# Performance work log

Measured on AMD Instinct MI355X. Metric: run time of the kernel, lower is better.

Reference implementation:

```python
import jax, jax.numpy as jnp
import numpy as np

N_BLADES = 8

def _build_cayley():
    """Geometric-product table for Cl(3,0): C[i,j,k] s.t. (e_i * e_j) = sum_k C[i,j,k] e_k.
    Blade order: [1, e1, e2, e3, e12, e13, e23, e123] via bitmasks [0,1,2,4,3,5,6,7]."""
    blades = [0, 1, 2, 4, 3, 5, 6, 7]
    idx = {b: i for i, b in enumerate(blades)}
    C = np.zeros((8, 8, 8), dtype=np.float32)
    for i, a in enumerate(blades):
        for j, b in enumerate(blades):
            aa = a >> 1
            cnt = 0
            while aa:
                cnt += bin(aa & b).count('1')
                aa >>= 1
            sign = -1.0 if (cnt & 1) else 1.0
            C[i, j, idx[a ^ b]] += sign
    return jnp.asarray(C)

CAYLEY = _build_cayley()

def clifford_linear(x, w, b):
    # x: (..., 8), w: (8,), b: (8,) -> geometric product w * x + b
    return jnp.einsum('ijk,i,...j->...k', CAYLEY, w, x) + b

def setup_inputs() -> dict:
    key = jax.random.key(0)
    ks = jax.random.split(key, 9)
    B, S = 4, 4096
    inp = {'x': jax.random.normal(ks[0], (B, S, N_BLADES), dtype=jnp.float32)}
    names = ['wq', 'bq', 'wk', 'bk', 'wv', 'bv', 'wo', 'bo']
    for i, n in enumerate(names):
        scale = 1.0 / np.sqrt(N_BLADES) if n.startswith('w') else 0.02
        inp[n] = jax.random.normal(ks[i + 1], (N_BLADES,), dtype=jnp.float32) * scale
    return inp

def reference(x, wq, bq, wk, bk, wv, bv, wo, bo):
    # head_dim = max(1, 8 // 2) = 4 -> scale = sqrt(4) = 2
    scale = jnp.float32(2.0)
    Q = clifford_linear(x, wq, bq)  # (B,S,8)
    K = clifford_linear(x, wk, bk)
    V = clifford_linear(x, wv, bv)
    c0 = CAYLEY[..., 0]  # (8,8) scalar part of geometric product
    attn = jnp.einsum('ij,bsi,btj->bst', c0, Q, K) / scale  # (B,S,S)
    attn = jax.nn.softmax(attn, axis=-1)
    out = jnp.einsum('bst,btk->bsk', attn, V)  # (B,S,8)
    return clifford_linear(out, wo, bo)
```

## Files before the change

### kernel.cpp

```cpp
#include <hip/hip_runtime.h>
#include <math.h>

#define SEQ 4096
#define NBATCH 4
#define SGRP 64
#define TWAVES 16
#define TCHUNK (SEQ / TWAVES)
#define TT 32
#define VTILE 288

typedef _Float16 f16;
typedef __attribute__((ext_vector_type(8))) _Float16 f16x8;
typedef __attribute__((ext_vector_type(8))) __bf16 bf16x8;
typedef __attribute__((ext_vector_type(16))) float f32x16;
typedef __attribute__((ext_vector_type(4))) unsigned u32x4;
typedef __attribute__((ext_vector_type(2))) unsigned u32x2;

__device__ __forceinline__ float fexp2(float x) {
#if __has_builtin(__builtin_amdgcn_exp2f)
  return __builtin_amdgcn_exp2f(x);
#else
  return exp2f(x);
#endif
}

__device__ __forceinline__ u32x2 pswap(unsigned a, unsigned b) {
#if __has_builtin(__builtin_amdgcn_permlane32_swap)
  return __builtin_amdgcn_permlane32_swap(a, b, false, false);
#else
  asm volatile("v_permlane32_swap_b32 %0, %1" : "+v"(a), "+v"(b));
  u32x2 r; r[0] = a; r[1] = b; return r;
#endif
}

__device__ __forceinline__ unsigned exp2_pk_bf16(float a, float b) {
  unsigned e0 = __builtin_bit_cast(unsigned, fexp2(a));
  unsigned e1 = __builtin_bit_cast(unsigned, fexp2(b));
  return __builtin_amdgcn_perm(e1, e0, 0x07060302u);
}

__device__ __forceinline__ unsigned short f2bf(float f) {
  unsigned u = __builtin_bit_cast(unsigned, f);
  u += 0x7FFF + ((u >> 16) & 1);
  return (unsigned short)(u >> 16);
}

__device__ __forceinline__ float cl_sign(int amask, int bmask) {
  int cnt = 0, aa = amask >> 1;
  while (aa) { cnt += __popc(aa & bmask); aa >>= 1; }
  return (cnt & 1) ? -1.f : 1.f;
}

__global__ __launch_bounds__(256) void ck_qkv(const float* __restrict__ x,
                                              const float* __restrict__ wq,
                                              const float* __restrict__ bq,
                                              const float* __restrict__ wk,
                                              const float* __restrict__ bk,
                                              const float* __restrict__ wv,
                                              const float* __restrict__ bv,
                                              f16* __restrict__ Qp,
                                              f16* __restrict__ Kp,
                                              unsigned short* __restrict__ Vt) {
  __shared__ float Pl[288];
  const int blades[8] = {0, 1, 2, 4, 3, 5, 6, 7};
  int tid = threadIdx.x;

  if (tid < 64) {
    int j = tid >> 3, k = tid & 7;
    int bj = blades[j];
    float mq = 0.f, mk = 0.f, mv = 0.f;
    for (int i = 0; i < 8; ++i) {
      int ai = blades[i];
      if (blades[ai ^ bj] != k) continue;
      float sgn = cl_sign(ai, bj);
      mq += sgn * wq[i]; mk += sgn * wk[i]; mv += sgn * wv[i];
    }
    float c0 = cl_sign(blades[k], blades[k]);
    const float F = 0.72134752044448170368f;
    Pl[tid]       = mq * c0 * F;
    Pl[64 + tid]  = mk;
    Pl[128 + tid] = mv;
    if (j == 0) {
      Pl[256 + k] = bq[k] * c0 * F;
      Pl[264 + k] = bk[k];
      Pl[272 + k] = bv[k];
    }
  }
  __syncthreads();

  int gid = blockIdx.x * 256 + tid;
  int row = gid >> 3;
  int c = gid & 7;
  int b = row >> 12;
  int s = row & (SEQ - 1);
  const float4* x4 = (const float4*)(x + (size_t)row * 8);
  float4 xa = x4[0], xb = x4[1];
  float xr[8] = {xa.x, xa.y, xa.z, xa.w, xb.x, xb.y, xb.z, xb.w};
  float q = Pl[256 + c], k = Pl[264 + c], v = Pl[272 + c];
#pragma unroll
  for (int j = 0; j < 8; ++j) {
    q = fmaf(xr[j], Pl[j * 8 + c], q);
    k = fmaf(xr[j], Pl[64 + j * 8 + c], k);
    v = fmaf(xr[j], Pl[128 + j * 8 + c], v);
  }
  f16 qh = (f16)q;
  f16 ql = (f16)(q - (float)qh);
  Qp[(size_t)row * 16 + c] = qh;
  Qp[(size_t)row * 16 + 8 + c] = ql;
  Kp[(size_t)row * 8 + c] = (f16)k;
  unsigned short* vt = Vt + ((size_t)b * (SEQ / 32) + (s >> 5)) * VTILE + (s & 31);
  vt[c * 32] = f2bf(v);
  if (c == 0) vt[8 * 32] = 0x3F80;
}

__global__ __launch_bounds__(1024, 4) void ck_attn(const f16* __restrict__ Qp,
                                                   const f16* __restrict__ Kp,
                                                   const unsigned short* __restrict__ Vt,
                                                   const float* __restrict__ wo,
                                                   const float* __restrict__ bo,
                                                   float* __restrict__ out) {
  __shared__ float Lo[TWAVES][SGRP][9];
  __shared__ float MoL[72];

  const int tid = threadIdx.x;
  const int w = tid >> 6;
  const int lane = tid & 63;
  const int ls = lane & 31;
  const int hf = lane >> 5;
  const int rowbase = blockIdx.x * SGRP;
  const int b = rowbase >> 12;

  if (tid < 64) {
    const int blades[8] = {0, 1, 2, 4, 3, 5, 6, 7};
    int j = tid >> 3, k = tid & 7;
    int bj = blades[j];
    float mo = 0.f;
    for (int i = 0; i < 8; ++i) {
      int ai = blades[i];
      if (blades[ai ^ bj] != k) continue;
      mo += cl_sign(ai, bj) * wo[i];
    }
    MoL[tid] = mo;
    if (j == 0) MoL[64 + k] = bo[k];
  }

  f16x8 qf0 = *(const f16x8*)(Qp + (size_t)(rowbase + ls) * 16 + 8 * hf);
  f16x8 qf1 = *(const f16x8*)(Qp + (size_t)(rowbase + 32 + ls) * 16 + 8 * hf);

  f32x16 acc0 = {0.f, 0.f, 0.f, 0.f, 0.f, 0.f, 0.f, 0.f,
                 0.f, 0.f, 0.f, 0.f, 0.f, 0.f, 0.f, 0.f};
  f32x16 acc1 = acc0;
  const f32x16 zero = acc0;

  const f16* kbase = Kp + ((size_t)b * SEQ + w * TCHUNK + ls) * 8;
  const unsigned short* vbase =
      Vt + ((size_t)b * (SEQ / 32) + w * (TCHUNK / 32)) * VTILE +
      (ls <= 8 ? ls : 8) * 32 + 8 * hf;

  const int NIT = TCHUNK / TT;

#pragma unroll 1
  for (int it = 0; it < NIT; ++it) {
    const int t0 = it * TT;
    f16x8 kf = *(const f16x8*)(kbase + (size_t)t0 * 8);
    u32x4 v0 = *(const u32x4*)(vbase + (size_t)it * VTILE);
    u32x4 v1 = *(const u32x4*)(vbase + (size_t)it * VTILE + 16);

    f32x16 s0 = __builtin_amdgcn_mfma_f32_32x32x16_f16(kf, qf0, zero, 0, 0, 0);
    f32x16 s1 = __builtin_amdgcn_mfma_f32_32x32x16_f16(kf, qf1, zero, 0, 0, 0);

    unsigned a0 = exp2_pk_bf16(s0[0], s0[1]);
    unsigned b0 = exp2_pk_bf16(s1[0], s1[1]);
    unsigned a1 = exp2_pk_bf16(s0[2], s0[3]);
    unsigned b1 = exp2_pk_bf16(s1[2], s1[3]);
    unsigned a2 = exp2_pk_bf16(s0[4], s0[5]);
    unsigned b2 = exp2_pk_bf16(s1[4], s1[5]);
    unsigned a3 = exp2_pk_bf16(s0[6], s0[7]);
    unsigned b3 = exp2_pk_bf16(s1[6], s1[7]);
    u32x2 ra02 = pswap(a0, a2);
    u32x2 rb02 = pswap(b0, b2);
    u32x2 ra13 = pswap(a1, a3);
    u32x2 rb13 = pswap(b1, b3);
    u32x4 pa0 = {ra02[0], ra13[0], ra02[1], ra13[1]};
    u32x4 pb0 = {rb02[0], rb13[0], rb02[1], rb13[1]};
    acc0 = __builtin_amdgcn_mfma_f32_32x32x16_bf16(
        __builtin_bit_cast(bf16x8, v0), __builtin_bit_cast(bf16x8, pa0), acc0, 0, 0, 0);
    acc1 = __builtin_amdgcn_mfma_f32_32x32x16_bf16(
        __builtin_bit_cast(bf16x8, v0), __builtin_bit_cast(bf16x8, pb0), acc1, 0, 0, 0);

    unsigned a4 = exp2_pk_bf16(s0[8], s0[9]);
    unsigned b4 = exp2_pk_bf16(s1[8], s1[9]);
    unsigned a5 = exp2_pk_bf16(s0[10], s0[11]);
    unsigned b5 = exp2_pk_bf16(s1[10], s1[11]);
    unsigned a6 = exp2_pk_bf16(s0[12], s0[13]);
    unsigned b6 = exp2_pk_bf16(s1[12], s1[13]);
    unsigned a7 = exp2_pk_bf16(s0[14], s0[15]);
    unsigned b7 = exp2_pk_bf16(s1[14], s1[15]);
    u32x2 ra46 = pswap(a4, a6);
    u32x2 rb46 = pswap(b4, b6);
    u32x2 ra57 = pswap(a5, a7);
    u32x2 rb57 = pswap(b5, b7);
    u32x4 pa1 = {ra46[0], ra57[0], ra46[1], ra57[1]};
    u32x4 pb1 = {rb46[0], rb57[0], rb46[1], rb57[1]};
    acc0 = __builtin_amdgcn_mfma_f32_32x32x16_bf16(
        __builtin_bit_cast(bf16x8, v1), __builtin_bit_cast(bf16x8, pa1), acc0, 0, 0, 0);
    acc1 = __builtin_amdgcn_mfma_f32_32x32x16_bf16(
        __builtin_bit_cast(bf16x8, v1), __builtin_bit_cast(bf16x8, pb1), acc1, 0, 0, 0);
  }

  if (hf == 0) {
    Lo[w][ls][0] = acc0[0]; Lo[w][ls][1] = acc0[1];
    Lo[w][ls][2] = acc0[2]; Lo[w][ls][3] = acc0[3];
    Lo[w][ls][8] = acc0[4];
    Lo[w][32 + ls][0] = acc1[0]; Lo[w][32 + ls][1] = acc1[1];
    Lo[w][32 + ls][2] = acc1[2]; Lo[w][32 + ls][3] = acc1[3];
    Lo[w][32 + ls][8] = acc1[4];
  } else {
    Lo[w][ls][4] = acc0[0]; Lo[w][ls][5] = acc0[1];
    Lo[w][ls][6] = acc0[2]; Lo[w][ls][7] = acc0[3];
    Lo[w][32 + ls][4] = acc1[0]; Lo[w][32 + ls][5] = acc1[1];
    Lo[w][32 + ls][6] = acc1[2]; Lo[w][32 + ls][7] = acc1[3];
  }
  __syncthreads();

  if (tid < SGRP * 9) {
    int s = tid / 9, j = tid - s * 9;
    float sum = 0.f;
#pragma unroll
    for (int w2 = 0; w2 < TWAVES; ++w2) sum += Lo[w2][s][j];
    Lo[0][s][j] = sum;
  }
  __syncthreads();

  if (tid < SGRP * 8) {
    int s = tid >> 3, ko = tid & 7;
    float inv = 1.f / Lo[0][s][8];
    float a = MoL[64 + ko];
#pragma unroll
    for (int j = 0; j < 8; ++j) a = fmaf(Lo[0][s][j] * inv, MoL[j * 8 + ko], a);
    out[(size_t)(rowbase + s) * 8 + ko] = a;
  }
}

extern "C" void kernel_launch(void* const* d_in, const int* in_sizes, int n_in,
                              void* d_out, int out_size, void* d_ws, size_t ws_size,
                              hipStream_t stream) {
  const float* x  = (const float*)d_in[0];
  const float* wq = (const float*)d_in[1];
  const float* bq = (const float*)d_in[2];
  const float* wk = (const float*)d_in[3];
  const float* bk = (const float*)d_in[4];
  const float* wv = (const float*)d_in[5];
  const float* bv = (const float*)d_in[6];
  const float* wo = (const float*)d_in[7];
  const float* bo = (const float*)d_in[8];

  f16* Qp = (f16*)d_ws;
  f16* Kp = Qp + (size_t)NBATCH * SEQ * 16;
  unsigned short* Vt = (unsigned short*)(Kp + (size_t)NBATCH * SEQ * 8);
  float* outp = (float*)d_out;

  hipLaunchKernelGGL(ck_qkv, dim3(NBATCH * SEQ * 8 / 256), dim3(256), 0, stream,
                     x, wq, bq, wk, bk, wv, bv, Qp, Kp, Vt);
  hipLaunchKernelGGL(ck_attn, dim3(NBATCH * SEQ / SGRP), dim3(1024), 0, stream,
                     Qp, Kp, Vt, wo, bo, outp);
}
```

Baseline: 21.02 us.

## Fuse QKV projection and attention into one cooperative kernel with grid sync

Merges the QKV projection kernel and the attention kernel into a single cooperative launch of 256 blocks. Each block first projects its own 64 rows into Q, K and V in the workspace, then waits on a grid-wide barrier before running attention. This removes one kernel launch and the gap between the two kernels. In exchange it adds the cost of a grid-wide sync and a cooperative launch, and it requires all 256 blocks of 1024 threads to be co-resident.

```diff
diff --git a/kernel.cpp b/kernel.cpp
--- a/kernel.cpp
+++ b/kernel.cpp
@@ -1,5 +1,8 @@
 #include <hip/hip_runtime.h>
+#include <hip/hip_cooperative_groups.h>
 #include <math.h>
+
+namespace cg = cooperative_groups;
 
 #define SEQ 4096
 #define NBATCH 4
@@ -8,6 +11,7 @@
 #define TCHUNK (SEQ / TWAVES)
 #define TT 32
 #define VTILE 288
+#define NGRP (NBATCH * SEQ / SGRP)
 
 typedef _Float16 f16;
 typedef __attribute__((ext_vector_type(8))) _Float16 f16x8;
@@ -51,98 +55,81 @@
   return (cnt & 1) ? -1.f : 1.f;
 }
 
-__global__ __launch_bounds__(256) void ck_qkv(const float* __restrict__ x,
-                                              const float* __restrict__ wq,
-                                              const float* __restrict__ bq,
-                                              const float* __restrict__ wk,
-                                              const float* __restrict__ bk,
-                                              const float* __restrict__ wv,
-                                              const float* __restrict__ bv,
-                                              f16* __restrict__ Qp,
-                                              f16* __restrict__ Kp,
-                                              unsigned short* __restrict__ Vt) {
+__global__ __launch_bounds__(1024, 4) void ck_fused(
+    const float* __restrict__ x,
+    const float* __restrict__ wq, const float* __restrict__ bq,
+    const float* __restrict__ wk, const float* __restrict__ bk,
+    const float* __restrict__ wv, const float* __restrict__ bv,
+    const float* __restrict__ wo, const float* __restrict__ bo,
+    f16* __restrict__ Qp, f16* __restrict__ Kp,
+    unsigned short* __restrict__ Vt, float* __restrict__ out) {
+  __shared__ float Lo[TWAVES][SGRP][9];
+  __shared__ float MoL[72];
   __shared__ float Pl[288];
+
+  const int tid = threadIdx.x;
   const int blades[8] = {0, 1, 2, 4, 3, 5, 6, 7};
-  int tid = threadIdx.x;
 
   if (tid < 64) {
     int j = tid >> 3, k = tid & 7;
     int bj = blades[j];
-    float mq = 0.f, mk = 0.f, mv = 0.f;
+    float mq = 0.f, mk = 0.f, mv = 0.f, mo = 0.f;
     for (int i = 0; i < 8; ++i) {
       int ai = blades[i];
       if (blades[ai ^ bj] != k) continue;
       float sgn = cl_sign(ai, bj);
-      mq += sgn * wq[i]; mk += sgn * wk[i]; mv += sgn * wv[i];
+      mq += sgn * wq[i]; mk += sgn * wk[i]; mv += sgn * wv[i]; mo += sgn * wo[i];
     }
     float c0 = cl_sign(blades[k], blades[k]);
     const float F = 0.72134752044448170368f;
     Pl[tid]       = mq * c0 * F;
     Pl[64 + tid]  = mk;
     Pl[128 + tid] = mv;
+    MoL[tid] = mo;
     if (j == 0) {
       Pl[256 + k] = bq[k] * c0 * F;
       Pl[264 + k] = bk[k];
       Pl[272 + k] = bv[k];
+      MoL[64 + k] = bo[k];
     }
   }
   __syncthreads();
 
-  int gid = blockIdx.x * 256 + tid;
-  int row = gid >> 3;
-  int c = gid & 7;
-  int b = row >> 12;
-  int s = row & (SEQ - 1);
-  const float4* x4 = (const float4*)(x + (size_t)row * 8);
-  float4 xa = x4[0], xb = x4[1];
-  float xr[8] = {xa.x, xa.y, xa.z, xa.w, xb.x, xb.y, xb.z, xb.w};
-  float q = Pl[256 + c], k = Pl[264 + c], v = Pl[272 + c];
+  const int rowbase = blockIdx.x * SGRP;
+
+  if (tid < 512) {
+    int row = rowbase + (tid >> 3);
+    int c = tid & 7;
+    int b_ = row >> 12;
+    int s = row & (SEQ - 1);
+    const float4* x4 = (const float4*)(x + (size_t)row * 8);
+    float4 xa = x4[0], xb = x4[1];
+    float xr[8] = {xa.x, xa.y, xa.z, xa.w, xb.x, xb.y, xb.z, xb.w};
+    float q = Pl[256 + c], k = Pl[264 + c], v = Pl[272 + c];
 #pragma unroll
-  for (int j = 0; j < 8; ++j) {
-    q = fmaf(xr[j], Pl[j * 8 + c], q);
-    k = fmaf(xr[j], Pl[64 + j * 8 + c], k);
-    v = fmaf(xr[j], Pl[128 + j * 8 + c], v);
-  }
-  f16 qh = (f16)q;
-  f16 ql = (f16)(q - (float)qh);
-  Qp[(size_t)row * 16 + c] = qh;
-  Qp[(size_t)row * 16 + 8 + c] = ql;
-  Kp[(size_t)row * 8 + c] = (f16)k;
-  unsigned short* vt = Vt + ((size_t)b * (SEQ / 32) + (s >> 5)) * VTILE + (s & 31);
-  vt[c * 32] = f2bf(v);
-  if (c == 0) vt[8 * 32] = 0x3F80;
-}
-
-__global__ __launch_bounds__(1024, 4) void ck_attn(const f16* __restrict__ Qp,
-                                                   const f16* __restrict__ Kp,
-                                                   const unsigned short* __restrict__ Vt,
-                                                   const float* __restrict__ wo,
-                                                   const float* __restrict__ bo,
-                                                   float* __restrict__ out) {
-  __shared__ float Lo[TWAVES][SGRP][9];
-  __shared__ float MoL[72];
-
-  const int tid = threadIdx.x;
+    for (int j = 0; j < 8; ++j) {
+      q = fmaf(xr[j], Pl[j * 8 + c], q);
+      k = fmaf(xr[j], Pl[64 + j * 8 + c], k);
+      v = fmaf(xr[j], Pl[128 + j * 8 + c], v);
+    }
+    f16 qh = (f16)q;
+    f16 ql = (f16)(q - (float)qh);
+    Qp[(size_t)row * 16 + c] = qh;
+    Qp[(size_t)row * 16 + 8 + c] = ql;
+    Kp[(size_t)row * 8 + c] = (f16)k;
+    unsigned short* vt =
+        Vt + ((size_t)b_ * (SEQ / 32) + (s >> 5)) * VTILE + (s & 31);
+    vt[c * 32] = f2bf(v);
+    if (c == 0) vt[8 * 32] = 0x3F80;
+  }
+
+  cg::this_grid().sync();
+
   const int w = tid >> 6;
   const int lane = tid & 63;
   const int ls = lane & 31;
   const int hf = lane >> 5;
-  const int rowbase = blockIdx.x * SGRP;
   const int b = rowbase >> 12;
-
-  if (tid < 64) {
-    const int blades[8] = {0, 1, 2, 4, 3, 5, 6, 7};
-    int j = tid >> 3, k = tid & 7;
-    int bj = blades[j];
-    float mo = 0.f;
-    for (int i = 0; i < 8; ++i) {
-      int ai = blades[i];
-      if (blades[ai ^ bj] != k) continue;
-      mo += cl_sign(ai, bj) * wo[i];
-    }
-    MoL[tid] = mo;
-    if (j == 0) MoL[64 + k] = bo[k];
-  }
 
   f16x8 qf0 = *(const f16x8*)(Qp + (size_t)(rowbase + ls) * 16 + 8 * hf);
   f16x8 qf1 = *(const f16x8*)(Qp + (size_t)(rowbase + 32 + ls) * 16 + 8 * hf);
@@ -260,8 +247,9 @@
   unsigned short* Vt = (unsigned short*)(Kp + (size_t)NBATCH * SEQ * 8);
   float* outp = (float*)d_out;
 
-  hipLaunchKernelGGL(ck_qkv, dim3(NBATCH * SEQ * 8 / 256), dim3(256), 0, stream,
-                     x, wq, bq, wk, bk, wv, bv, Qp, Kp, Vt);
-  hipLaunchKernelGGL(ck_attn, dim3(NBATCH * SEQ / SGRP), dim3(1024), 0, stream,
-                     Qp, Kp, Vt, wo, bo, outp);
-}
+  void* args[] = {(void*)&x,  (void*)&wq, (void*)&bq, (void*)&wk, (void*)&bk,
+                  (void*)&wv, (void*)&bv, (void*)&wo, (void*)&bo,
+                  (void*)&Qp, (void*)&Kp, (void*)&Vt, (void*)&outp};
+  hipLaunchCooperativeKernel((void*)ck_fused, dim3(NGRP), dim3(1024), args, 0,
+                             stream);
+}
```

New measurement: 61.86 us. 2.94x slower.
